# Kernel optimization log

Hardware: AMD Instinct MI355X
Metric: run time of the kernel (lower is better)

## Reference

```python
import jax, jax.numpy as jnp
import numpy as np

B = 16384      # batch_size
G = 8          # max_groups (groups per batch element in this setup)
P = G * (G - 1) // 2   # 28 docking pairs
D = 128        # node_dim
DG = 128       # global_dim
N = B * G      # num_nodes


def setup_inputs() -> dict:
    key = jax.random.key(0)
    ks = jax.random.split(key, 10)
    node_features = jax.random.normal(ks[0], (N, D), dtype=jnp.float32)
    global_features = jax.random.normal(ks[1], (B, DG), dtype=jnp.float32)
    # every node is a group; exactly G groups per batch element, sorted batch ids
    group_mask = jnp.ones((N,), dtype=bool)
    batch = jnp.repeat(jnp.arange(B, dtype=jnp.int32), G)
    docking_valid_mask = jax.random.bernoulli(ks[2], 0.8, (B, P))
    # pair_scorer: Linear(384,128) -> ReLU -> Linear(128,64) -> ReLU -> Linear(64,1)
    W1 = jax.random.normal(ks[3], (2 * D + DG, 128), dtype=jnp.float32) * 0.05
    b1 = jax.random.normal(ks[4], (128,), dtype=jnp.float32) * 0.05
    W2 = jax.random.normal(ks[5], (128, 64), dtype=jnp.float32) * 0.05
    b2 = jax.random.normal(ks[6], (64,), dtype=jnp.float32) * 0.05
    W3 = jax.random.normal(ks[7], (64, 1), dtype=jnp.float32) * 0.05
    b3 = jax.random.normal(ks[8], (1,), dtype=jnp.float32) * 0.05
    return {
        "node_features": node_features,
        "global_features": global_features,
        "group_mask": group_mask,
        "docking_valid_mask": docking_valid_mask,
        "batch": batch,
        "W1": W1, "b1": b1, "W2": W2, "b2": b2, "W3": W3, "b3": b3,
    }


def reference(node_features, global_features, group_mask, docking_valid_mask,
              batch, W1, b1, W2, b2, W3, b3):
    # Setup guarantees group_mask is all-True and `batch` is sorted with exactly
    # G groups per batch element, so the per-batch group gathering in the original
    # nested loop reduces to a reshape. Pair enumeration order (i outer, j inner)
    # matches np.triu_indices row-major order.
    Bsz, Dg = global_features.shape
    groups = node_features.reshape(Bsz, G, -1)          # [B, G, D]
    iu, ju = np.triu_indices(G, k=1)                    # P pairs, loop order
    gi = groups[:, iu]                                  # [B, P, D]
    gj = groups[:, ju]                                  # [B, P, D]
    gf = jnp.broadcast_to(global_features[:, None, :], (Bsz, P, Dg))
    x = jnp.concatenate([gi, gj, gf], axis=-1)          # [B, P, 2D+DG]
    h = jax.nn.relu(x @ W1 + b1)
    h = jax.nn.relu(h @ W2 + b2)
    scores = (h @ W3 + b3)[..., 0]                      # [B, P]
    NEG = jnp.float32(-1e9)
    return jnp.where(docking_valid_mask, scores, NEG)
```

## Files before the change

kernel.cpp:

```cpp
#include <hip/hip_runtime.h>

typedef float    v4f    __attribute__((ext_vector_type(4)));
typedef __fp16   f16x8  __attribute__((ext_vector_type(8)));
typedef __fp16   f16x2  __attribute__((ext_vector_type(2)));
typedef short    bf16x8 __attribute__((ext_vector_type(8)));
typedef unsigned u32x4  __attribute__((ext_vector_type(4)));
typedef unsigned short u16;

__constant__ unsigned char c_pair[28] = {
  1,2,3,4,5,6,7, 10,11,12,13,14,15, 19,20,21,22,23, 28,29,30,31, 37,38,39, 46,47, 55
};

static __device__ __forceinline__ unsigned asu(float f){ union{float f;unsigned u;}v; v.f=f; return v.u; }
static __device__ __forceinline__ float lo2f(unsigned d){ union{unsigned u;float f;}v; v.u = d<<16; return v.f; }
static __device__ __forceinline__ float hi2f(unsigned d){ union{unsigned u;float f;}v; v.u = d & 0xffff0000u; return v.f; }
static __device__ __forceinline__ unsigned pkt(float lo, float hi){
  return __builtin_amdgcn_perm(asu(hi), asu(lo), 0x07060302u);
}
static __device__ __forceinline__ unsigned pkh(float lo, float hi){
  union { f16x2 h; unsigned u; } v;
  v.h = __builtin_amdgcn_cvt_pkrtz(lo, hi);
  return v.u;
}

#define WS_W1AB 0
#define WS_W1G  65536
#define WS_W2   98304
#define WS_GP   114688
#define WS_NEED 4308992

__global__ __launch_bounds__(1024)
void prep_weights(const float* __restrict__ W1, const float* __restrict__ W2, char* __restrict__ ws)
{
  const int idx = blockIdx.x * 1024 + threadIdx.x;
  if (idx < 16384) {
    const int c = idx >> 6, kp = idx & 63;
    const int part = c >> 7, cc = c & 127;
    const float a  = W1[(size_t)(part * 128 + 2 * kp) * 128 + cc];
    const float b_ = W1[(size_t)(part * 128 + 2 * kp + 1) * 128 + cc];
    *(unsigned*)(ws + WS_W1AB + (size_t)c * 256 + ((kp * 4) ^ ((c & 7) << 4))) = pkh(a, b_);
  } else if (idx < 24576) {
    const int j = idx - 16384, c = j >> 6, kp = j & 63;
    const float a  = W1[(size_t)(256 + 2 * kp) * 128 + c];
    const float b_ = W1[(size_t)(256 + 2 * kp + 1) * 128 + c];
    *(unsigned*)(ws + WS_W1G + (size_t)c * 256 + ((kp * 4) ^ ((c & 7) << 4))) = pkh(a, b_);
  } else if (idx < 28672) {
    const int j = idx - 24576, c = j >> 6, kp = j & 63;
    const float a  = W2[(size_t)(2 * kp) * 64 + c];
    const float b_ = W2[(size_t)(2 * kp + 1) * 64 + c];
    *(unsigned*)(ws + WS_W2 + (size_t)c * 256 + ((kp * 4) ^ ((c & 7) << 4))) = pkh(a, b_);
  }
}

__global__ __launch_bounds__(256)
void prep_gp(const float* __restrict__ glob, const float* __restrict__ b1, char* __restrict__ ws)
{
  __shared__ __align__(16) char sm[65536];
  const int tid = threadIdx.x;
  const int bb0 = blockIdx.x * 128;
  for (int i = tid; i < 2048; i += 256) {
    const u32x4 v = *(const u32x4*)(ws + WS_W1G + i * 16);
    *(u32x4*)(sm + 32768 + i * 16) = v;
  }
  for (int i = tid; i < 4096; i += 256) {
    const int r = i >> 5, q = i & 31;
    const float4 f = *(const float4*)(glob + (size_t)(bb0 + r) * 128 + q * 4);
    int2 w; w.x = (int)pkh(f.x, f.y); w.y = (int)pkh(f.z, f.w);
    *(int2*)(sm + r * 256 + ((q * 8) ^ ((r & 7) << 4))) = w;
  }
  __syncthreads();
  const int wave = tid >> 6, lane = tid & 63, lrow = lane & 15, lko = (lane >> 4) * 8;
  float b1c[8];
#pragma unroll
  for (int nt = 0; nt < 8; ++nt) b1c[nt] = b1[nt * 16 + lrow];
  const v4f vzero = {0.f, 0.f, 0.f, 0.f};
  v4f acc[2][8];
#pragma unroll
  for (int mt = 0; mt < 2; ++mt)
#pragma unroll
    for (int nt = 0; nt < 8; ++nt) acc[mt][nt] = vzero;
#pragma unroll
  for (int ks = 0; ks < 4; ++ks) {
    const int kb = (ks * 32 + lko) * 2;
    f16x8 af[2];
#pragma unroll
    for (int mt = 0; mt < 2; ++mt) {
      const int r = wave * 32 + mt * 16 + lrow;
      af[mt] = *(const f16x8*)(sm + r * 256 + (kb ^ ((r & 7) << 4)));
    }
#pragma unroll
    for (int nt = 0; nt < 8; ++nt) {
      const int c = nt * 16 + lrow;
      const f16x8 bfr = *(const f16x8*)(sm + 32768 + c * 256 + (kb ^ ((c & 7) << 4)));
#pragma unroll
      for (int mt = 0; mt < 2; ++mt)
        acc[mt][nt] = __builtin_amdgcn_mfma_f32_16x16x32_f16(af[mt], bfr, acc[mt][nt], 0, 0, 0);
    }
  }
#pragma unroll
  for (int mt = 0; mt < 2; ++mt)
#pragma unroll
    for (int nt = 0; nt < 8; ++nt) {
      const int c = nt * 16 + lrow;
#pragma unroll
      for (int rg = 0; rg < 4; ++rg) {
        const int m = wave * 32 + mt * 16 + (lane >> 4) * 4 + rg;
        const int batch = bb0 + m;
        const int g = batch >> 4, q = m & 15;
        *(u16*)(ws + WS_GP + (size_t)g * 4096 + q * 256 + ((c * 2) ^ ((q & 7) << 4))) =
            (u16)pkh(acc[mt][nt][rg] + b1c[nt], 0.0f);
      }
    }
}

#define M3_ND   0
#define M3_PA   16384
#define M3_PB   32768
#define M3_GP   49152
#define M3_V    53248
#define M3_SMEM 53760

__global__ __launch_bounds__(512)
void docking_main(const float* __restrict__ node, const int* __restrict__ dmask,
                  const float* __restrict__ b2, const float* __restrict__ W3,
                  const float* __restrict__ b3,
                  const char* __restrict__ ws, float* __restrict__ outp)
{
  __shared__ __align__(16) char smem[M3_SMEM];
  const int tid = threadIdx.x;
  const int wave = tid >> 6, lane = tid & 63, lrow = lane & 15, lko = (lane >> 4) * 8;
  const int wm = wave >> 2, wn = wave & 3;
  const int bb0 = blockIdx.x * 8;
  const float bias3 = *b3;
  const v4f vzero = {0.f, 0.f, 0.f, 0.f};
  const char* wsW = ws + WS_W1AB;
  const char* wsW2 = ws + WS_W2;
  const int pbase = (wn >= 2) ? M3_PB : M3_PA;

  for (int idx = tid; idx < 64 * 32; idx += 512) {
    const int r = idx >> 5, q = idx & 31;
    const float4 f = *(const float4*)(node + ((size_t)bb0 * 8 + r) * 128 + q * 4);
    int2 w; w.x = (int)pkh(f.x, f.y); w.y = (int)pkh(f.z, f.w);
    *(int2*)(smem + M3_ND + r * 256 + ((q * 8) ^ ((r & 7) << 4))) = w;
  }
  {
    const int q = tid >> 6, cp = tid & 63;
    const int qq = (bb0 & 15) + q;
    union { unsigned u; f16x2 h; } cv;
    cv.u = *(const unsigned*)(ws + WS_GP + ((size_t)(bb0 >> 4)) * 4096
                              + qq * 256 + ((cp * 4) ^ ((qq & 7) << 4)));
    float* gq = (float*)(smem + M3_GP) + q * 128;
    gq[cp * 2] = (float)cv.h[0]; gq[cp * 2 + 1] = (float)cv.h[1];
  }
  if (tid < 64)       ((float*)(smem + M3_V))[tid] = b2[tid];
  else if (tid < 128) ((float*)(smem + M3_V))[tid] = W3[tid - 64];
  __syncthreads();

  v4f acc[2][4];
#pragma unroll
  for (int mt = 0; mt < 2; ++mt)
#pragma unroll
    for (int nt = 0; nt < 4; ++nt) acc[mt][nt] = vzero;

#pragma unroll
  for (int ks = 0; ks < 4; ++ks) {
    const int kb = (ks * 32 + lko) * 2;
    f16x8 Bf[4];
#pragma unroll
    for (int nt = 0; nt < 4; ++nt) {
      const int c = wn * 64 + nt * 16 + lrow;
      Bf[nt] = *(const f16x8*)(wsW + c * 256 + (kb ^ ((c & 7) << 4)));
    }
#pragma unroll
    for (int mt = 0; mt < 2; ++mt) {
      const int rr = wm * 32 + mt * 16 + lrow;
      const f16x8 Af = *(const f16x8*)(smem + M3_ND + rr * 256 + (kb ^ ((rr & 7) << 4)));
#pragma unroll
      for (int nt = 0; nt < 4; ++nt)
        acc[mt][nt] = __builtin_amdgcn_mfma_f32_16x16x32_f16(Bf[nt], Af, acc[mt][nt], 0, 0, 0);
    }
  }
#pragma unroll
  for (int mt = 0; mt < 2; ++mt) {
    const int m = wm * 32 + mt * 16 + lrow;
#pragma unroll
    for (int nt = 0; nt < 4; ++nt) {
      const int cb = (wn & 1) * 64 + nt * 16 + (lane >> 4) * 4;
      float v0 = acc[mt][nt][0], v1 = acc[mt][nt][1];
      float v2 = acc[mt][nt][2], v3 = acc[mt][nt][3];
      if (wn >= 2) {
        const float4 g = *(const float4*)((const float*)(smem + M3_GP) + (m >> 3) * 128 + cb);
        v0 += g.x; v1 += g.y; v2 += g.z; v3 += g.w;
      }
      int2 w; w.x = (int)pkh(v0, v1); w.y = (int)pkh(v2, v3);
      *(int2*)(smem + pbase + m * 256 + ((cb * 2) ^ ((m & 7) << 4))) = w;
    }
  }
  __syncthreads();

  const float* sV = (const float*)(smem + M3_V);
  for (int t = wave; t < 14; t += 8) {
    const int r  = t * 16 + lrow;
    const int bb = (r * 9363) >> 18;
    const int p  = r - bb * 28;
    const unsigned pr8 = c_pair[p];
    const int mi = bb * 8 + (int)(pr8 >> 3);
    const int mj = bb * 8 + (int)(pr8 & 7);

    v4f acc2[4] = {vzero, vzero, vzero, vzero};
#pragma unroll
    for (int ks = 0; ks < 4; ++ks) {
      const int kb = (ks * 32 + lko) * 2;
      const f16x8 va = *(const f16x8*)(smem + M3_PA + mi * 256 + (kb ^ ((mi & 7) << 4)));
      const f16x8 vb = *(const f16x8*)(smem + M3_PB + mj * 256 + (kb ^ ((mj & 7) << 4)));
      f16x8 h1 = va + vb;
      h1 = __builtin_elementwise_max(h1, (f16x8)(__fp16)0.0f);
#pragma unroll
      for (int nt = 0; nt < 4; ++nt) {
        const int cc = nt * 16 + lrow;
        const f16x8 w2fr = *(const f16x8*)(wsW2 + cc * 256 + (kb ^ ((cc & 7) << 4)));
        acc2[nt] = __builtin_amdgcn_mfma_f32_16x16x32_f16(h1, w2fr, acc2[nt], 0, 0, 0);
      }
    }
    float part[4] = {0.f, 0.f, 0.f, 0.f};
#pragma unroll
    for (int nt = 0; nt < 4; ++nt) {
      const int n = nt * 16 + lrow;
      const float b2v = sV[n], w3v = sV[64 + n];
#pragma unroll
      for (int rg = 0; rg < 4; ++rg)
        part[rg] += fmaxf(acc2[nt][rg] + b2v, 0.0f) * w3v;
    }
#pragma unroll
    for (int mk = 1; mk < 16; mk <<= 1)
#pragma unroll
      for (int rg = 0; rg < 4; ++rg) part[rg] += __shfl_xor(part[rg], mk, 16);

    if ((lane & 15) == 0) {
      const int rb = t * 16 + (lane >> 4) * 4;
#pragma unroll
      for (int rg = 0; rg < 4; ++rg) {
        const int rr = rb + rg;
        const int b2_ = (rr * 9363) >> 18;
        const int p2  = rr - b2_ * 28;
        const size_t o = (size_t)(bb0 + b2_) * 28 + p2;
        outp[o] = dmask[o] ? (part[rg] + bias3) : -1.0e9f;
      }
    }
  }
}

#define F_THREADS 512
#define F_NB      8
#define F_OFF_A    0
#define F_OFF_GL   16384
#define F_OFF_SB   20480
#define F_OFF_W2   53248
#define F_OFF_B1V  69632
#define F_OFF_B2V  70144
#define F_OFF_W3V  70400
#define F_SMEM     70656

__global__ __launch_bounds__(F_THREADS, 4)
void docking_fused(const float* __restrict__ node, const float* __restrict__ glob,
                   const int* __restrict__ dmask,
                   const float* __restrict__ W1, const float* __restrict__ b1,
                   const float* __restrict__ W2, const float* __restrict__ b2,
                   const float* __restrict__ W3, const float* __restrict__ b3,
                   float* __restrict__ outp)
{
  __shared__ __align__(16) char smem[F_SMEM];
  const int tid = threadIdx.x;
  const int bb0 = blockIdx.x * F_NB;
  const size_t nrow0 = (size_t)bb0 * 8;
  const float bias3 = *b3;

  if (tid < 128)      ((float*)(smem + F_OFF_B1V))[tid]       = b1[tid];
  else if (tid < 192) ((float*)(smem + F_OFF_B2V))[tid - 128] = b2[tid - 128];
  else if (tid < 256) ((float*)(smem + F_OFF_W3V))[tid - 192] = W3[tid - 192];

  for (int idx = tid; idx < 64 * 32; idx += F_THREADS) {
    const int r = idx >> 5, q = idx & 31;
    const float4 f = *(const float4*)(node + (nrow0 + (size_t)r) * 128 + q * 4);
    int2 w; w.x = (int)pkt(f.x, f.y); w.y = (int)pkt(f.z, f.w);
    *(int2*)(smem + F_OFF_A + r * 256 + ((q * 8) ^ ((r & 7) << 4))) = w;
  }
  for (int idx = tid; idx < 16 * 32; idx += F_THREADS) {
    const int r = idx >> 5, q = idx & 31;
    float4 f = make_float4(0.f, 0.f, 0.f, 0.f);
    if (r < F_NB) f = *(const float4*)(glob + (size_t)(bb0 + r) * 128 + q * 4);
    int2 w; w.x = (int)pkt(f.x, f.y); w.y = (int)pkt(f.z, f.w);
    *(int2*)(smem + F_OFF_GL + r * 256 + ((q * 8) ^ ((r & 7) << 4))) = w;
  }
  for (int idx = tid; idx < 4096; idx += F_THREADS) {
    const int cl = idx & 7, kl = (idx >> 3) & 7, ch = (idx >> 6) & 7, kh = idx >> 9;
    const int c = cl | (ch << 3), kp = kl | (kh << 3);
    const float a  = W2[(size_t)(2 * kp) * 64 + c];
    const float b_ = W2[(size_t)(2 * kp + 1) * 64 + c];
    *(unsigned*)(smem + F_OFF_W2 + c * 256 + ((kp * 4) ^ ((c & 7) << 4))) = pkt(a, b_);
  }
  auto stageB = [&](int rowOff) {
    for (int idx = tid; idx < 8192; idx += F_THREADS) {
      const int cl = idx & 7, kl = (idx >> 3) & 7, ch = (idx >> 6) & 15, kh = idx >> 10;
      const int c = cl | (ch << 3), kp = kl | (kh << 3);
      const float a  = W1[(size_t)(rowOff + 2 * kp) * 128 + c];
      const float b_ = W1[(size_t)(rowOff + 2 * kp + 1) * 128 + c];
      *(unsigned*)(smem + F_OFF_SB + c * 256 + ((kp * 4) ^ ((c & 7) << 4))) = pkt(a, b_);
    }
  };
  stageB(0);
  __syncthreads();

  const int wave = tid >> 6, lane = tid & 63;
  const int lrow = lane & 15;
  const int lko  = (lane >> 4) * 8;
  const int wmt = wave >> 1, wnh = wave & 1;
  const v4f vzero = {0.f, 0.f, 0.f, 0.f};

  bf16x8 af[4];
#pragma unroll
  for (int ks = 0; ks < 4; ++ks) {
    const int r = wmt * 16 + lrow;
    af[ks] = *(const bf16x8*)(smem + F_OFF_A + r * 256 + (((ks * 32 + lko) * 2) ^ ((r & 7) << 4)));
  }
  v4f acc_a[4] = {vzero, vzero, vzero, vzero};
#pragma unroll
  for (int ks = 0; ks < 4; ++ks) {
    const int kb = (ks * 32 + lko) * 2;
#pragma unroll
    for (int nt = 0; nt < 4; ++nt) {
      const int c = wnh * 64 + nt * 16 + lrow;
      const bf16x8 bfr = *(const bf16x8*)(smem + F_OFF_SB + c * 256 + (kb ^ ((c & 7) << 4)));
      acc_a[nt] = __builtin_amdgcn_mfma_f32_16x16x32_bf16(af[ks], bfr, acc_a[nt], 0, 0, 0);
    }
  }
  __syncthreads();
  stageB(128);
  __syncthreads();
  v4f acc_b[4] = {vzero, vzero, vzero, vzero};
#pragma unroll
  for (int ks = 0; ks < 4; ++ks) {
    const int kb = (ks * 32 + lko) * 2;
#pragma unroll
    for (int nt = 0; nt < 4; ++nt) {
      const int c = wnh * 64 + nt * 16 + lrow;
      const bf16x8 bfr = *(const bf16x8*)(smem + F_OFF_SB + c * 256 + (kb ^ ((c & 7) << 4)));
      acc_b[nt] = __builtin_amdgcn_mfma_f32_16x16x32_bf16(af[ks], bfr, acc_b[nt], 0, 0, 0);
    }
  }
  __syncthreads();
  stageB(256);
  __syncthreads();
  v4f accg = vzero;
#pragma unroll
  for (int ks = 0; ks < 4; ++ks) {
    const int kb = (ks * 32 + lko) * 2;
    const bf16x8 ag = *(const bf16x8*)(smem + F_OFF_GL + lrow * 256 + (kb ^ ((lrow & 7) << 4)));
    const int cg = wave * 16 + lrow;
    const bf16x8 bg = *(const bf16x8*)(smem + F_OFF_SB + cg * 256 + (kb ^ ((cg & 7) << 4)));
    accg = __builtin_amdgcn_mfma_f32_16x16x32_bf16(ag, bg, accg, 0, 0, 0);
  }
  __syncthreads();
  {
    const int rgb = (lane >> 4) * 4;
#pragma unroll
    for (int nt = 0; nt < 4; ++nt) {
      const int c = wnh * 64 + nt * 16 + lrow;
#pragma unroll
      for (int rg = 0; rg < 4; ++rg) {
        const int m = wmt * 16 + rgb + rg;
        const int sw = (c * 2) ^ ((m & 7) << 4);
        *(u16*)(smem + F_OFF_SB + m * 256 + sw)        = (u16)(asu(acc_a[nt][rg]) >> 16);
        *(u16*)(smem + F_OFF_SB + (64 + m) * 256 + sw) = (u16)(asu(acc_b[nt][rg]) >> 16);
      }
    }
    const int cg = wave * 16 + lrow;
    const float b1c = ((const float*)(smem + F_OFF_B1V))[cg];
#pragma unroll
    for (int rg = 0; rg < 4; ++rg) {
      const int bbr = rgb + rg;
      if (bbr < F_NB)
        *(u16*)(smem + F_OFF_A + bbr * 256 + ((cg * 2) ^ ((bbr & 7) << 4))) =
            (u16)(asu(accg[rg] + b1c) >> 16);
    }
  }
  __syncthreads();

  float b2n[4], w3n[4];
#pragma unroll
  for (int nt = 0; nt < 4; ++nt) {
    const int n = nt * 16 + lrow;
    b2n[nt] = ((const float*)(smem + F_OFF_B2V))[n];
    w3n[nt] = ((const float*)(smem + F_OFF_W3V))[n];
  }
  for (int t = wave; t < 14; t += 8) {
    const int r  = t * 16 + lrow;
    const int bb = (r * 9363) >> 18;
    const int p  = r - bb * 28;
    const unsigned pr8 = c_pair[p];
    const int mi = bb * 8 + (int)(pr8 >> 3);
    const int mj = 64 + bb * 8 + (int)(pr8 & 7);
    v4f acc2[4] = {vzero, vzero, vzero, vzero};
#pragma unroll
    for (int ks = 0; ks < 4; ++ks) {
      const int kb = (ks * 32 + lko) * 2;
      const u32x4 va = *(const u32x4*)(smem + F_OFF_SB + mi * 256 + (kb ^ ((mi & 7) << 4)));
      const u32x4 vb = *(const u32x4*)(smem + F_OFF_SB + mj * 256 + (kb ^ ((mj & 7) << 4)));
      const u32x4 vg = *(const u32x4*)(smem + F_OFF_A  + bb * 256 + (kb ^ ((bb & 7) << 4)));
      u32x4 a2;
#pragma unroll
      for (int w = 0; w < 4; ++w) {
        const float lo = fmaxf(lo2f(va[w]) + lo2f(vb[w]) + lo2f(vg[w]), 0.0f);
        const float hi = fmaxf(hi2f(va[w]) + hi2f(vb[w]) + hi2f(vg[w]), 0.0f);
        a2[w] = pkt(lo, hi);
      }
      union { u32x4 u; bf16x8 h; } cv; cv.u = a2;
#pragma unroll
      for (int nt = 0; nt < 4; ++nt) {
        const int c = nt * 16 + lrow;
        const bf16x8 w2fr = *(const bf16x8*)(smem + F_OFF_W2 + c * 256 + (kb ^ ((c & 7) << 4)));
        acc2[nt] = __builtin_amdgcn_mfma_f32_16x16x32_bf16(cv.h, w2fr, acc2[nt], 0, 0, 0);
      }
    }
    float part[4] = {0.f, 0.f, 0.f, 0.f};
#pragma unroll
    for (int nt = 0; nt < 4; ++nt)
#pragma unroll
      for (int rg = 0; rg < 4; ++rg)
        part[rg] += fmaxf(acc2[nt][rg] + b2n[nt], 0.0f) * w3n[nt];
#pragma unroll
    for (int mk = 1; mk < 16; mk <<= 1)
#pragma unroll
      for (int rg = 0; rg < 4; ++rg) part[rg] += __shfl_xor(part[rg], mk, 16);
    if ((lane & 15) == 0) {
      const int rb = t * 16 + (lane >> 4) * 4;
#pragma unroll
      for (int rg = 0; rg < 4; ++rg) {
        const int rr = rb + rg;
        const int b2_ = (rr * 9363) >> 18;
        const int p2  = rr - b2_ * 28;
        const size_t o = (size_t)(bb0 + b2_) * 28 + p2;
        outp[o] = dmask[o] ? (part[rg] + bias3) : -1.0e9f;
      }
    }
  }
}

extern "C" void kernel_launch(void* const* d_in, const int* in_sizes, int n_in,
                              void* d_out, int out_size, void* d_ws, size_t ws_size,
                              hipStream_t stream) {
  (void)in_sizes; (void)n_in; (void)out_size;
  const float* node = (const float*)d_in[0];
  const float* glob = (const float*)d_in[1];
  const int* dmsk   = (const int*)d_in[3];
  const float* W1 = (const float*)d_in[5];
  const float* b1 = (const float*)d_in[6];
  const float* W2 = (const float*)d_in[7];
  const float* b2 = (const float*)d_in[8];
  const float* W3 = (const float*)d_in[9];
  const float* b3 = (const float*)d_in[10];
  float* outp = (float*)d_out;

  if (ws_size >= (size_t)WS_NEED) {
    char* ws = (char*)d_ws;
    prep_weights<<<28, 1024, 0, stream>>>(W1, W2, ws);
    prep_gp<<<128, 256, 0, stream>>>(glob, b1, ws);
    docking_main<<<2048, 512, 0, stream>>>(node, dmsk, b2, W3, b3, ws, outp);
  } else {
    docking_fused<<<16384 / F_NB, F_THREADS, 0, stream>>>(node, glob, dmsk, W1, b1, W2, b2, W3, b3, outp);
  }
}
```

Baseline: 63.02 us.

## Fuse global-feature projection into main kernel and shrink shared memory

Result: faster. 55.39 us, median of 2 (-12.1%).

```diff
diff --git a/kernel.cpp b/kernel.cpp
--- a/kernel.cpp
+++ b/kernel.cpp
@@ -26,8 +26,7 @@
 #define WS_W1AB 0
 #define WS_W1G  65536
 #define WS_W2   98304
-#define WS_GP   114688
-#define WS_NEED 4308992
+#define WS_NEED 114688
 
 __global__ __launch_bounds__(1024)
 void prep_weights(const float* __restrict__ W1, const float* __restrict__ W2, char* __restrict__ ws)
@@ -52,108 +51,47 @@
   }
 }
 
-__global__ __launch_bounds__(256)
-void prep_gp(const float* __restrict__ glob, const float* __restrict__ b1, char* __restrict__ ws)
-{
-  __shared__ __align__(16) char sm[65536];
-  const int tid = threadIdx.x;
-  const int bb0 = blockIdx.x * 128;
-  for (int i = tid; i < 2048; i += 256) {
-    const u32x4 v = *(const u32x4*)(ws + WS_W1G + i * 16);
-    *(u32x4*)(sm + 32768 + i * 16) = v;
-  }
-  for (int i = tid; i < 4096; i += 256) {
-    const int r = i >> 5, q = i & 31;
-    const float4 f = *(const float4*)(glob + (size_t)(bb0 + r) * 128 + q * 4);
-    int2 w; w.x = (int)pkh(f.x, f.y); w.y = (int)pkh(f.z, f.w);
-    *(int2*)(sm + r * 256 + ((q * 8) ^ ((r & 7) << 4))) = w;
-  }
-  __syncthreads();
-  const int wave = tid >> 6, lane = tid & 63, lrow = lane & 15, lko = (lane >> 4) * 8;
-  float b1c[8];
-#pragma unroll
-  for (int nt = 0; nt < 8; ++nt) b1c[nt] = b1[nt * 16 + lrow];
-  const v4f vzero = {0.f, 0.f, 0.f, 0.f};
-  v4f acc[2][8];
-#pragma unroll
-  for (int mt = 0; mt < 2; ++mt)
-#pragma unroll
-    for (int nt = 0; nt < 8; ++nt) acc[mt][nt] = vzero;
-#pragma unroll
-  for (int ks = 0; ks < 4; ++ks) {
-    const int kb = (ks * 32 + lko) * 2;
-    f16x8 af[2];
-#pragma unroll
-    for (int mt = 0; mt < 2; ++mt) {
-      const int r = wave * 32 + mt * 16 + lrow;
-      af[mt] = *(const f16x8*)(sm + r * 256 + (kb ^ ((r & 7) << 4)));
-    }
-#pragma unroll
-    for (int nt = 0; nt < 8; ++nt) {
-      const int c = nt * 16 + lrow;
-      const f16x8 bfr = *(const f16x8*)(sm + 32768 + c * 256 + (kb ^ ((c & 7) << 4)));
-#pragma unroll
-      for (int mt = 0; mt < 2; ++mt)
-        acc[mt][nt] = __builtin_amdgcn_mfma_f32_16x16x32_f16(af[mt], bfr, acc[mt][nt], 0, 0, 0);
-    }
-  }
-#pragma unroll
-  for (int mt = 0; mt < 2; ++mt)
-#pragma unroll
-    for (int nt = 0; nt < 8; ++nt) {
-      const int c = nt * 16 + lrow;
-#pragma unroll
-      for (int rg = 0; rg < 4; ++rg) {
-        const int m = wave * 32 + mt * 16 + (lane >> 4) * 4 + rg;
-        const int batch = bb0 + m;
-        const int g = batch >> 4, q = m & 15;
-        *(u16*)(ws + WS_GP + (size_t)g * 4096 + q * 256 + ((c * 2) ^ ((q & 7) << 4))) =
-            (u16)pkh(acc[mt][nt][rg] + b1c[nt], 0.0f);
-      }
-    }
-}
-
-#define M3_ND   0
-#define M3_PA   16384
-#define M3_PB   32768
-#define M3_GP   49152
-#define M3_V    53248
-#define M3_SMEM 53760
+#define M4_ND   0
+#define M4_PB   16384
+#define M4_GP   32768
+#define M4_V    36864
+#define M4_SMEM 37888
 
 __global__ __launch_bounds__(512)
-void docking_main(const float* __restrict__ node, const int* __restrict__ dmask,
-                  const float* __restrict__ b2, const float* __restrict__ W3,
-                  const float* __restrict__ b3,
+void docking_main(const float* __restrict__ node, const float* __restrict__ glob,
+                  const int* __restrict__ dmask,
+                  const float* __restrict__ b1, const float* __restrict__ b2,
+                  const float* __restrict__ W3, const float* __restrict__ b3,
                   const char* __restrict__ ws, float* __restrict__ outp)
 {
-  __shared__ __align__(16) char smem[M3_SMEM];
+  __shared__ __align__(16) char smem[M4_SMEM];
   const int tid = threadIdx.x;
   const int wave = tid >> 6, lane = tid & 63, lrow = lane & 15, lko = (lane >> 4) * 8;
   const int wm = wave >> 2, wn = wave & 3;
   const int bb0 = blockIdx.x * 8;
   const float bias3 = *b3;
   const v4f vzero = {0.f, 0.f, 0.f, 0.f};
-  const char* wsW = ws + WS_W1AB;
+  const char* wsW  = ws + WS_W1AB;
+  const char* wsWg = ws + WS_W1G;
   const char* wsW2 = ws + WS_W2;
-  const int pbase = (wn >= 2) ? M3_PB : M3_PA;
+  float* sV = (float*)(smem + M4_V);
 
   for (int idx = tid; idx < 64 * 32; idx += 512) {
     const int r = idx >> 5, q = idx & 31;
     const float4 f = *(const float4*)(node + ((size_t)bb0 * 8 + r) * 128 + q * 4);
     int2 w; w.x = (int)pkh(f.x, f.y); w.y = (int)pkh(f.z, f.w);
-    *(int2*)(smem + M3_ND + r * 256 + ((q * 8) ^ ((r & 7) << 4))) = w;
+    *(int2*)(smem + M4_ND + r * 256 + ((q * 8) ^ ((r & 7) << 4))) = w;
   }
   {
-    const int q = tid >> 6, cp = tid & 63;
-    const int qq = (bb0 & 15) + q;
-    union { unsigned u; f16x2 h; } cv;
-    cv.u = *(const unsigned*)(ws + WS_GP + ((size_t)(bb0 >> 4)) * 4096
-                              + qq * 256 + ((cp * 4) ^ ((qq & 7) << 4)));
-    float* gq = (float*)(smem + M3_GP) + q * 128;
-    gq[cp * 2] = (float)cv.h[0]; gq[cp * 2 + 1] = (float)cv.h[1];
-  }
-  if (tid < 64)       ((float*)(smem + M3_V))[tid] = b2[tid];
-  else if (tid < 128) ((float*)(smem + M3_V))[tid] = W3[tid - 64];
+    const int r = tid >> 5, q = tid & 31;
+    float4 f = make_float4(0.f, 0.f, 0.f, 0.f);
+    if (r < 8) f = *(const float4*)(glob + ((size_t)bb0 + r) * 128 + q * 4);
+    int2 w; w.x = (int)pkh(f.x, f.y); w.y = (int)pkh(f.z, f.w);
+    *(int2*)(smem + M4_PB + r * 256 + ((q * 8) ^ ((r & 7) << 4))) = w;
+  }
+  if (tid < 128)      sV[tid] = b1[tid];
+  else if (tid < 192) sV[64 + tid] = b2[tid - 128];
+  else if (tid < 256) sV[64 + tid] = W3[tid - 192];
   __syncthreads();
 
   v4f acc[2][4];
@@ -174,12 +112,33 @@
 #pragma unroll
     for (int mt = 0; mt < 2; ++mt) {
       const int rr = wm * 32 + mt * 16 + lrow;
-      const f16x8 Af = *(const f16x8*)(smem + M3_ND + rr * 256 + (kb ^ ((rr & 7) << 4)));
+      const f16x8 Af = *(const f16x8*)(smem + M4_ND + rr * 256 + (kb ^ ((rr & 7) << 4)));
 #pragma unroll
       for (int nt = 0; nt < 4; ++nt)
         acc[mt][nt] = __builtin_amdgcn_mfma_f32_16x16x32_f16(Bf[nt], Af, acc[mt][nt], 0, 0, 0);
     }
   }
+  {
+    v4f accg = vzero;
+#pragma unroll
+    for (int ks = 0; ks < 4; ++ks) {
+      const int kb = (ks * 32 + lko) * 2;
+      const f16x8 ag = *(const f16x8*)(smem + M4_PB + lrow * 256 + (kb ^ ((lrow & 7) << 4)));
+      const int cg = wave * 16 + lrow;
+      const f16x8 bg = *(const f16x8*)(wsWg + cg * 256 + (kb ^ ((cg & 7) << 4)));
+      accg = __builtin_amdgcn_mfma_f32_16x16x32_f16(ag, bg, accg, 0, 0, 0);
+    }
+    const int cg = wave * 16 + lrow;
+    const float b1c = sV[cg];
+    const int q0 = (lane >> 4) * 4;
+    if (q0 < 8) {
+#pragma unroll
+      for (int rg = 0; rg < 4; ++rg)
+        ((float*)(smem + M4_GP))[(q0 + rg) * 128 + cg] = accg[rg] + b1c;
+    }
+  }
+  __syncthreads();
+
 #pragma unroll
   for (int mt = 0; mt < 2; ++mt) {
     const int m = wm * 32 + mt * 16 + lrow;
@@ -189,16 +148,16 @@
       float v0 = acc[mt][nt][0], v1 = acc[mt][nt][1];
       float v2 = acc[mt][nt][2], v3 = acc[mt][nt][3];
       if (wn >= 2) {
-        const float4 g = *(const float4*)((const float*)(smem + M3_GP) + (m >> 3) * 128 + cb);
+        const float4 g = *(const float4*)((const float*)(smem + M4_GP) + (m >> 3) * 128 + cb);
         v0 += g.x; v1 += g.y; v2 += g.z; v3 += g.w;
       }
       int2 w; w.x = (int)pkh(v0, v1); w.y = (int)pkh(v2, v3);
-      *(int2*)(smem + pbase + m * 256 + ((cb * 2) ^ ((m & 7) << 4))) = w;
-    }
-  }
-  __syncthreads();
-
-  const float* sV = (const float*)(smem + M3_V);
+      const int pb = (wn >= 2) ? M4_PB : M4_ND;
+      *(int2*)(smem + pb + m * 256 + ((cb * 2) ^ ((m & 7) << 4))) = w;
+    }
+  }
+  __syncthreads();
+
   for (int t = wave; t < 14; t += 8) {
     const int r  = t * 16 + lrow;
     const int bb = (r * 9363) >> 18;
@@ -211,8 +170,8 @@
 #pragma unroll
     for (int ks = 0; ks < 4; ++ks) {
       const int kb = (ks * 32 + lko) * 2;
-      const f16x8 va = *(const f16x8*)(smem + M3_PA + mi * 256 + (kb ^ ((mi & 7) << 4)));
-      const f16x8 vb = *(const f16x8*)(smem + M3_PB + mj * 256 + (kb ^ ((mj & 7) << 4)));
+      const f16x8 va = *(const f16x8*)(smem + M4_ND + mi * 256 + (kb ^ ((mi & 7) << 4)));
+      const f16x8 vb = *(const f16x8*)(smem + M4_PB + mj * 256 + (kb ^ ((mj & 7) << 4)));
       f16x8 h1 = va + vb;
       h1 = __builtin_elementwise_max(h1, (f16x8)(__fp16)0.0f);
 #pragma unroll
@@ -226,7 +185,7 @@
 #pragma unroll
     for (int nt = 0; nt < 4; ++nt) {
       const int n = nt * 16 + lrow;
-      const float b2v = sV[n], w3v = sV[64 + n];
+      const float b2v = sV[192 + n], w3v = sV[256 + n];
 #pragma unroll
       for (int rg = 0; rg < 4; ++rg)
         part[rg] += fmaxf(acc2[nt][rg] + b2v, 0.0f) * w3v;
@@ -464,8 +423,7 @@
   if (ws_size >= (size_t)WS_NEED) {
     char* ws = (char*)d_ws;
     prep_weights<<<28, 1024, 0, stream>>>(W1, W2, ws);
-    prep_gp<<<128, 256, 0, stream>>>(glob, b1, ws);
-    docking_main<<<2048, 512, 0, stream>>>(node, dmsk, b2, W3, b3, ws, outp);
+    docking_main<<<2048, 512, 0, stream>>>(node, glob, dmsk, b1, b2, W3, b3, ws, outp);
   } else {
     docking_fused<<<16384 / F_NB, F_THREADS, 0, stream>>>(node, glob, dmsk, W1, b1, W2, b2, W3, b3, outp);
   }
```
